# Kernel tuning notes

Measured on AMD Instinct MI355X. Metric: run time of the kernel, lower is better.

## Reference

```python
import jax, jax.numpy as jnp
import numpy as np

H = 1024

def setup_inputs() -> dict:
    key = jax.random.key(0)
    ks = jax.random.split(key, 7)
    s = 1.0 / np.sqrt(H)
    return {
        "hidden_states": jax.random.normal(ks[0], (4, 2048, H), dtype=jnp.float32),
        "Wq": jax.random.uniform(ks[1], (H, H), jnp.float32, -s, s),
        "bq": jax.random.uniform(ks[2], (H,), jnp.float32, -s, s),
        "Wk": jax.random.uniform(ks[3], (H, H), jnp.float32, -s, s),
        "bk": jax.random.uniform(ks[4], (H,), jnp.float32, -s, s),
        "Wv": jax.random.uniform(ks[5], (H, H), jnp.float32, -s, s),
        "bv": jax.random.uniform(ks[6], (H,), jnp.float32, -s, s),
    }

def reference(hidden_states, Wq, bq, Wk, bk, Wv, bv):
    # Linear projections (torch Linear: x @ W.T + b)
    q = hidden_states @ Wq.T + bq  # [B,S,H]
    k = hidden_states @ Wk.T + bk
    v = hidden_states @ Wv.T + bv
    # Unscaled attention
    probs = jax.nn.softmax(jnp.einsum("bqh,bkh->bqk", q, k), axis=-1)  # [B,S,S]
    attention_scores = jnp.sum(probs, axis=-2)  # [B,S] column sums
    context = jnp.einsum("bqk,bkh->bqh", probs, v)  # [B,S,H]
    return (context, attention_scores)
```

## Files before the change

### kernel.cpp

```cpp
#include <hip/hip_runtime.h>
#include <stdint.h>


typedef __attribute__((ext_vector_type(8))) short short8;
typedef __attribute__((ext_vector_type(4))) float floatx4;
typedef __attribute__((ext_vector_type(4))) unsigned short ushort4v;
typedef __attribute__((ext_vector_type(8))) unsigned short ushort8v;
typedef unsigned short u16;

__device__ __forceinline__ u16 f2bf(float f) {
  union { float f; uint32_t u; } v; v.f = f;
  uint32_t u = v.u;
  return (u16)((u + 0x7FFFu + ((u >> 16) & 1u)) >> 16);
}
__device__ __forceinline__ float bf2f(u16 h) {
  union { uint32_t u; float f; } v; v.u = ((uint32_t)h) << 16; return v.f;
}

#define AS3(p) ((__attribute__((address_space(3))) void*)(uint32_t)(uintptr_t)(p))
#define AS1(p) ((__attribute__((address_space(1))) void*)(uintptr_t)(p))

__global__ __launch_bounds__(256) void cvt_all_kernel(
    const float* __restrict__ hs, const float* __restrict__ Wq,
    const float* __restrict__ Wk, const float* __restrict__ Wv,
    u16* __restrict__ hsb, u16* __restrict__ Wb, float* __restrict__ lsum) {
  const int bx = blockIdx.x;
  const float* src;
  u16* dst;
  int i;
  if (bx < 4096) {
    i = bx * 2048 + threadIdx.x * 8;
    src = hs; dst = hsb;
  } else {
    const int idx = bx - 4096;
    const int p = idx >> 9, blk = idx & 511;
    src = (p == 0) ? Wq : (p == 1) ? Wk : Wv;
    dst = Wb + p * 1048576;
    i = blk * 2048 + threadIdx.x * 8;
  }
  const float4 v0 = *(const float4*)(src + i);
  const float4 v1 = *(const float4*)(src + i + 4);
  ushort8v o;
  o[0] = f2bf(v0.x); o[1] = f2bf(v0.y); o[2] = f2bf(v0.z); o[3] = f2bf(v0.w);
  o[4] = f2bf(v1.x); o[5] = f2bf(v1.y); o[6] = f2bf(v1.z); o[7] = f2bf(v1.w);
  *(ushort8v*)(dst + i) = o;
  if (bx == 0) {
    float4 z = {0.f, 0.f, 0.f, 0.f};
#pragma unroll
    for (int k = 0; k < 8; ++k)
      *(float4*)(lsum + threadIdx.x * 32 + k * 4) = z;
  }
}

#define DC_SLOTU 24576

template <int NT>
__device__ __forceinline__ void deep_core(const u16* __restrict__ A,
                                          const u16* __restrict__ B,
                                          int lda, int ldb,
                                          u16* smem, floatx4 acc[4][4]) {
  const int tid  = threadIdx.x;
  const int lane = tid & 63;
  const int w    = tid >> 6;
  const int wm   = w >> 1;
  const int wn   = w & 1;
  const int fr   = lane & 15;
  const int quad = lane >> 4;
  const int pc0  = (quad ^ (fr & 7)) * 8;
  const int pc1  = ((4 + quad) ^ (fr & 7)) * 8;

  const u16* pA[4]; uint32_t dA[4];
#pragma unroll
  for (int j = 0; j < 4; ++j) {
    const int c = tid + j * 512, row = c >> 3, kc = c & 7;
    pA[j] = A + row * lda + (kc ^ (row & 7)) * 8;
    dA[j] = c * 8;
  }
  const u16* pB[2]; uint32_t dB[2];
#pragma unroll
  for (int j = 0; j < 2; ++j) {
    const int c = tid + j * 512, row = c >> 3, kc = c & 7;
    pB[j] = B + row * ldb + (kc ^ (row & 7)) * 8;
    dB[j] = 16384 + c * 8;
  }

#define DC_STA(u) do { u16* s_ = smem + ((u) % 3) * DC_SLOTU;                                  \
    _Pragma("unroll") for (int j_ = 0; j_ < 4; ++j_)                                           \
      __builtin_amdgcn_global_load_lds(AS1(pA[j_] + (u) * 64), AS3(s_ + dA[j_]), 16, 0, 0);   \
  } while (0)
#define DC_STB(u) do { u16* s_ = smem + ((u) % 3) * DC_SLOTU;                                  \
    _Pragma("unroll") for (int j_ = 0; j_ < 2; ++j_)                                           \
      __builtin_amdgcn_global_load_lds(AS1(pB[j_] + (u) * 64), AS3(s_ + dB[j_]), 16, 0, 0);   \
  } while (0)

  DC_STA(0); DC_STB(0); DC_STA(1); DC_STB(1);
  asm volatile("s_waitcnt vmcnt(6)" ::: "memory");
  __builtin_amdgcn_s_barrier();

  const int arow0 = wm * 64 + fr;
  const int brow0 = wn * 64 + fr;

#pragma unroll
  for (int t = 0; t < NT; ++t) {
    const u16* sA = smem + (t % 3) * DC_SLOTU;
    const u16* sB = sA + 16384;
    short8 af[4], bf[4];

#pragma unroll
    for (int mi = 0; mi < 4; ++mi)
      af[mi] = *(const short8*)(sA + (arow0 + mi * 16) * 64 + pc0);
#pragma unroll
    for (int ni = 0; ni < 4; ++ni)
      bf[ni] = *(const short8*)(sB + (brow0 + ni * 16) * 64 + pc0);
    if (t < NT - 2) DC_STA(t + 2);
    __builtin_amdgcn_s_barrier();
    asm volatile("s_waitcnt lgkmcnt(0)" ::: "memory");
    __builtin_amdgcn_sched_barrier(0);
    __builtin_amdgcn_s_setprio(1);
#pragma unroll
    for (int mi = 0; mi < 4; ++mi)
#pragma unroll
      for (int ni = 0; ni < 4; ++ni)
        acc[mi][ni] = __builtin_amdgcn_mfma_f32_16x16x32_bf16(af[mi], bf[ni],
                                                              acc[mi][ni], 0, 0, 0);
    __builtin_amdgcn_s_setprio(0);
    __builtin_amdgcn_s_barrier();

#pragma unroll
    for (int mi = 0; mi < 4; ++mi)
      af[mi] = *(const short8*)(sA + (arow0 + mi * 16) * 64 + pc1);
#pragma unroll
    for (int ni = 0; ni < 4; ++ni)
      bf[ni] = *(const short8*)(sB + (brow0 + ni * 16) * 64 + pc1);
    if (t < NT - 2) {
      DC_STB(t + 2);
      asm volatile("s_waitcnt vmcnt(6)" ::: "memory");
    } else if (t == NT - 2) {
      asm volatile("s_waitcnt vmcnt(0)" ::: "memory");
    }
    __builtin_amdgcn_s_barrier();
    asm volatile("s_waitcnt lgkmcnt(0)" ::: "memory");
    __builtin_amdgcn_sched_barrier(0);
    __builtin_amdgcn_s_setprio(1);
#pragma unroll
    for (int mi = 0; mi < 4; ++mi)
#pragma unroll
      for (int ni = 0; ni < 4; ++ni)
        acc[mi][ni] = __builtin_amdgcn_mfma_f32_16x16x32_bf16(af[mi], bf[ni],
                                                              acc[mi][ni], 0, 0, 0);
    __builtin_amdgcn_s_setprio(0);
    __builtin_amdgcn_s_barrier();
  }
#undef DC_STA
#undef DC_STB
}

__global__ __launch_bounds__(512, 2) void proj_deep_kernel(
    const u16* __restrict__ hsb, const u16* __restrict__ Wb,
    const float* __restrict__ bq, const float* __restrict__ bk,
    const float* __restrict__ bv,
    u16* __restrict__ qo, u16* __restrict__ ko, u16* __restrict__ vt) {
  extern __shared__ __align__(16) u16 smem[];
  floatx4 acc[4][4];
#pragma unroll
  for (int i = 0; i < 4; ++i)
#pragma unroll
    for (int j = 0; j < 4; ++j) acc[i][j] = {0.f, 0.f, 0.f, 0.f};

  const int p    = blockIdx.z;
  const int flat = blockIdx.x + blockIdx.y * 8;
  const int swz  = (flat & 7) * 32 + (flat >> 3);
  const int m0   = (swz >> 3) * 256;
  const int n0   = (swz & 7) * 128;

  deep_core<16>(hsb + m0 * 1024, Wb + p * 1048576 + n0 * 1024, 1024, 1024, smem, acc);

  const float* bias = (p == 0) ? bq : (p == 1) ? bk : bv;
  const int lane = threadIdx.x & 63, w = threadIdx.x >> 6;
  const int wm = w >> 1, wn = w & 1;
  const int fr = lane & 15, rg4 = (lane >> 4) * 4;

  if (p < 2) {
    u16* out = (p == 0) ? qo : ko;
#pragma unroll
    for (int mi = 0; mi < 4; ++mi)
#pragma unroll
      for (int ni = 0; ni < 4; ++ni) {
        const int n = n0 + wn * 64 + ni * 16 + fr;
        const float bn = bias[n];
#pragma unroll
        for (int r = 0; r < 4; ++r) {
          const int m = m0 + wm * 64 + mi * 16 + rg4 + r;
          out[m * 1024 + n] = f2bf(acc[mi][ni][r] + bn);
        }
      }
  } else {
#pragma unroll
    for (int mi = 0; mi < 4; ++mi) {
      const int mbase = m0 + wm * 64 + mi * 16 + rg4;
      const int b = mbase >> 11, s = mbase & 2047;
#pragma unroll
      for (int ni = 0; ni < 4; ++ni) {
        const int n = n0 + wn * 64 + ni * 16 + fr;
        const float bn = bias[n];
        ushort4v pk;
#pragma unroll
        for (int r = 0; r < 4; ++r) pk[r] = f2bf(acc[mi][ni][r] + bn);
        *(ushort4v*)(vt + b * 2097152 + n * 2048 + s) = pk;
      }
    }
  }
}

__global__ __launch_bounds__(512, 2) void logits_q4_kernel(
    const u16* __restrict__ q, const u16* __restrict__ k,
    u16* __restrict__ E, float* __restrict__ lsum) {
  extern __shared__ __align__(16) u16 smem[];
  const int tid  = threadIdx.x;
  const int lane = tid & 63;
  const int w    = tid >> 6;
  const int wr4  = w >> 2;
  const int wc4  = w & 3;
  const int fr   = lane & 15;
  const int kq   = lane >> 4;
  const int pc0  = (kq ^ (fr & 7)) * 8;
  const int pc1  = ((4 + kq) ^ (fr & 7)) * 8;

  const int flat = blockIdx.x + blockIdx.y * 8 + blockIdx.z * 64;
  const int swz  = (flat & 7) * 32 + (flat >> 3);
  const int b    = swz >> 6;
  const int m0   = ((swz >> 3) & 7) * 256;
  const int n0   = (swz & 7) * 256;

  const u16* Ag = q + (b * 2048 + m0) * 1024;
  const u16* Bg = k + (b * 2048 + n0) * 1024;

  const u16* pAs[2]; const u16* pBs[2]; uint32_t dof[2];
#pragma unroll
  for (int j = 0; j < 2; ++j) {
    const int c = tid + j * 512, rl = c >> 3, kc = c & 7;
    const int gc = (kc ^ (rl & 7)) * 8;
    pAs[j] = Ag + rl * 1024 + gc;
    pBs[j] = Bg + rl * 1024 + gc;
    dof[j] = c * 8;
  }
#define ST_A(h, tt, sbase) do { _Pragma("unroll") for (int j_ = 0; j_ < 2; ++j_)      \
    __builtin_amdgcn_global_load_lds(AS1(pAs[j_] + (h) * 131072 + (tt) * 64),         \
        AS3(smem + (sbase) + (h) * 8192 + dof[j_]), 16, 0, 0); } while (0)
#define ST_B(h, tt, sbase) do { _Pragma("unroll") for (int j_ = 0; j_ < 2; ++j_)      \
    __builtin_amdgcn_global_load_lds(AS1(pBs[j_] + (h) * 131072 + (tt) * 64),         \
        AS3(smem + (sbase) + 16384 + (h) * 8192 + dof[j_]), 16, 0, 0); } while (0)

  floatx4 acc[2][2][4][2];
#pragma unroll
  for (int i = 0; i < 2; ++i)
#pragma unroll
    for (int j = 0; j < 2; ++j)
#pragma unroll
      for (int mi = 0; mi < 4; ++mi)
#pragma unroll
        for (int ni = 0; ni < 2; ++ni) acc[i][j][mi][ni] = {0.f, 0.f, 0.f, 0.f};

  ST_A(0, 0, 0); ST_B(0, 0, 0); ST_B(1, 0, 0); ST_A(1, 0, 0);
  asm volatile("s_waitcnt vmcnt(4)" ::: "memory");
  __builtin_amdgcn_s_barrier();

  const int ar0 = wr4 * 64 + fr;
  const int br0 = wc4 * 32 + fr;
  short8 af[4][2], bf[2][2];

#define Q4_READ_A(ah) do { _Pragma("unroll") for (int mi = 0; mi < 4; ++mi) {          \
    af[mi][0] = *(const short8*)(sA + ((ah) * 128 + ar0 + mi * 16) * 64 + pc0);        \
    af[mi][1] = *(const short8*)(sA + ((ah) * 128 + ar0 + mi * 16) * 64 + pc1); } } while (0)
#define Q4_READ_B(bh) do { _Pragma("unroll") for (int ni = 0; ni < 2; ++ni) {          \
    bf[ni][0] = *(const short8*)(sB + ((bh) * 128 + br0 + ni * 16) * 64 + pc0);        \
    bf[ni][1] = *(const short8*)(sB + ((bh) * 128 + br0 + ni * 16) * 64 + pc1); } } while (0)
#define Q4_MFMA(ah, bh) do {                                                           \
    __builtin_amdgcn_s_barrier();                                                      \
    asm volatile("s_waitcnt lgkmcnt(0)" ::: "memory");                                 \
    __builtin_amdgcn_sched_barrier(0);                                                 \
    __builtin_amdgcn_s_setprio(1);                                                     \
    _Pragma("unroll") for (int mi = 0; mi < 4; ++mi)                                   \
      _Pragma("unroll") for (int ni = 0; ni < 2; ++ni)                                 \
        _Pragma("unroll") for (int ks = 0; ks < 2; ++ks)                               \
          acc[ah][bh][mi][ni] = __builtin_amdgcn_mfma_f32_16x16x32_bf16(               \
              af[mi][ks], bf[ni][ks], acc[ah][bh][mi][ni], 0, 0, 0);                   \
    __builtin_amdgcn_s_setprio(0);                                                     \
    __builtin_amdgcn_s_barrier(); } while (0)

  for (int t = 0; t < 15; ++t) {
    const uint32_t sb = (uint32_t)(t & 1) * 32768u;
    const uint32_t sn = (uint32_t)((t + 1) & 1) * 32768u;
    const u16* sA = smem + sb;
    const u16* sB = sA + 16384;

    Q4_READ_A(0); Q4_READ_B(0);
    ST_A(0, t + 1, sn);
    asm volatile("s_waitcnt vmcnt(4)" ::: "memory");
    Q4_MFMA(0, 0);
    Q4_READ_B(1);
    ST_B(0, t + 1, sn);
    asm volatile("s_waitcnt vmcnt(4)" ::: "memory");
    Q4_MFMA(0, 1);
    Q4_READ_A(1); Q4_READ_B(0);
    ST_B(1, t + 1, sn);
    Q4_MFMA(1, 0);
    Q4_READ_B(1);
    ST_A(1, t + 1, sn);
    asm volatile("s_waitcnt vmcnt(4)" ::: "memory");
    Q4_MFMA(1, 1);
  }

  {
    const u16* sA = smem + 32768;
    const u16* sB = sA + 16384;
    Q4_READ_A(0); Q4_READ_B(0);
    asm volatile("s_waitcnt vmcnt(2)" ::: "memory");
    Q4_MFMA(0, 0);
    Q4_READ_B(1);
    asm volatile("s_waitcnt vmcnt(0)" ::: "memory");
    Q4_MFMA(0, 1);
    Q4_READ_A(1); Q4_READ_B(0);
    Q4_MFMA(1, 0);
    Q4_READ_B(1);
    Q4_MFMA(1, 1);
  }

  u16* Eb = E + b * 4194304;
  float* lb = lsum + b * 2048;
#pragma unroll
  for (int ah = 0; ah < 2; ++ah)
#pragma unroll
    for (int mi = 0; mi < 4; ++mi) {
      floatx4 rs = {0.f, 0.f, 0.f, 0.f};
      const int rbase = m0 + ah * 128 + wr4 * 64 + mi * 16 + kq * 4;
#pragma unroll
      for (int bh = 0; bh < 2; ++bh)
#pragma unroll
        for (int ni = 0; ni < 2; ++ni) {
          const int n = n0 + bh * 128 + wc4 * 32 + ni * 16 + fr;
#pragma unroll
          for (int r = 0; r < 4; ++r) {
            const float e = __expf(acc[ah][bh][mi][ni][r]);
            rs[r] += e;
            Eb[(rbase + r) * 2048 + n] = f2bf(e);
          }
        }
#pragma unroll
      for (int off = 1; off < 16; off <<= 1) {
        rs[0] += __shfl_xor(rs[0], off, 64);
        rs[1] += __shfl_xor(rs[1], off, 64);
        rs[2] += __shfl_xor(rs[2], off, 64);
        rs[3] += __shfl_xor(rs[3], off, 64);
      }
      if (fr == 0) {
#pragma unroll
        for (int r = 0; r < 4; ++r) atomicAdd(&lb[rbase + r], rs[r]);
      }
    }
#undef Q4_READ_A
#undef Q4_READ_B
#undef Q4_MFMA
#undef ST_A
#undef ST_B
}

__global__ __launch_bounds__(512, 2) void context_deep_kernel(
    const u16* __restrict__ E, const u16* __restrict__ vt,
    const float* __restrict__ lsum, float* __restrict__ out) {
  extern __shared__ __align__(16) u16 smem[];
  floatx4 acc[4][4];
#pragma unroll
  for (int i = 0; i < 4; ++i)
#pragma unroll
    for (int j = 0; j < 4; ++j) acc[i][j] = {0.f, 0.f, 0.f, 0.f};

  const int flat = blockIdx.x + blockIdx.y * 8 + blockIdx.z * 64;
  const int swz  = (flat & 7) * 32 + (flat >> 3);
  const int b    = swz >> 6;
  const int m0   = ((swz >> 3) & 7) * 256;
  const int n0   = (swz & 7) * 128;

  deep_core<32>(E + b * 4194304 + m0 * 2048, vt + b * 2097152 + n0 * 2048,
                2048, 2048, smem, acc);

  const int lane = threadIdx.x & 63, w = threadIdx.x >> 6;
  const int wm = w >> 1, wn = w & 1;
  const int fr = lane & 15, rg4 = (lane >> 4) * 4;
  const float* lb = lsum + b * 2048;

#pragma unroll
  for (int mi = 0; mi < 4; ++mi) {
    const int rbase = m0 + wm * 64 + mi * 16 + rg4;
    float rinv[4];
#pragma unroll
    for (int r = 0; r < 4; ++r) rinv[r] = 1.0f / lb[rbase + r];
#pragma unroll
    for (int ni = 0; ni < 4; ++ni) {
      const int n = n0 + wn * 64 + ni * 16 + fr;
#pragma unroll
      for (int r = 0; r < 4; ++r)
        out[(b * 2048 + rbase + r) * 1024 + n] = acc[mi][ni][r] * rinv[r];
    }
  }
}

__global__ __launch_bounds__(256) void colsum_part_kernel(
    const u16* __restrict__ E, const float* __restrict__ lsum,
    float* __restrict__ part) {
  const int b  = blockIdx.x;
  const int g  = blockIdx.y;
  const int q0 = g * 64;
  const int j  = blockIdx.z * 1024 + threadIdx.x * 4;
  const u16* Eb = E + b * 4194304;
  const float* lb = lsum + b * 2048;
  float acc[4];
#pragma unroll
  for (int c = 0; c < 4; ++c) acc[c] = 0.f;
  for (int r = 0; r < 64; ++r) {
    const int qi = q0 + r;
    const float rinv = 1.0f / lb[qi];
    const ushort4v ev = *(const ushort4v*)(Eb + qi * 2048 + j);
#pragma unroll
    for (int c = 0; c < 4; ++c) acc[c] += bf2f((u16)ev[c]) * rinv;
  }
  float4 o = {acc[0], acc[1], acc[2], acc[3]};
  *(float4*)(part + (b * 32 + g) * 2048 + j) = o;
}

__global__ __launch_bounds__(256) void colsum_reduce_kernel(
    const float* __restrict__ part, float* __restrict__ scores) {
  const int b = blockIdx.x;
  const int j = blockIdx.y * 256 + threadIdx.x;
  const float* pb = part + b * 32 * 2048 + j;
  float s = 0.f;
#pragma unroll
  for (int g = 0; g < 32; ++g) s += pb[g * 2048];
  scores[b * 2048 + j] = s;
}

extern "C" void kernel_launch(void* const* d_in, const int* in_sizes, int n_in,
                              void* d_out, int out_size, void* d_ws, size_t ws_size,
                              hipStream_t stream) {
  const float* hs = (const float*)d_in[0];
  const float* Wq = (const float*)d_in[1];
  const float* bq = (const float*)d_in[2];
  const float* Wk = (const float*)d_in[3];
  const float* bk = (const float*)d_in[4];
  const float* Wv = (const float*)d_in[5];
  const float* bv = (const float*)d_in[6];

  char* ws = (char*)d_ws;
  u16*   qw  = (u16*)(ws);
  u16*   kw  = (u16*)(ws + (16u << 20));
  u16*   vtw = (u16*)(ws + (32u << 20));
  float* lw  = (float*)(ws + (48u << 20));
  float* pw  = (float*)(ws + (48u << 20) + (128u << 10));
  u16*   hsb = (u16*)(ws + (49u << 20));
  u16*   Wb  = (u16*)(ws + (65u << 20));
  u16*   Ew  = (u16*)(ws + (49u << 20));

  float* outc = (float*)d_out;
  float* outs = outc + 8388608;

  static int s_attr_done = 0;
  if (!s_attr_done) {
    (void)hipFuncSetAttribute((const void*)proj_deep_kernel,
                              hipFuncAttributeMaxDynamicSharedMemorySize, 147456);
    (void)hipFuncSetAttribute((const void*)logits_q4_kernel,
                              hipFuncAttributeMaxDynamicSharedMemorySize, 131072);
    (void)hipFuncSetAttribute((const void*)context_deep_kernel,
                              hipFuncAttributeMaxDynamicSharedMemorySize, 147456);
    s_attr_done = 1;
  }

  cvt_all_kernel<<<5632, 256, 0, stream>>>(hs, Wq, Wk, Wv, hsb, Wb, lw);
  proj_deep_kernel<<<dim3(8, 32, 3), 512, 147456, stream>>>(hsb, Wb, bq, bk, bv, qw, kw, vtw);
  logits_q4_kernel<<<dim3(8, 8, 4), 512, 131072, stream>>>(qw, kw, Ew, lw);
  context_deep_kernel<<<dim3(8, 8, 4), 512, 147456, stream>>>(Ew, vtw, lw, outc);
  colsum_part_kernel<<<dim3(4, 32, 2), 256, 0, stream>>>(Ew, lw, pw);
  colsum_reduce_kernel<<<dim3(4, 8), 256, 0, stream>>>(pw, outs);
}
```

Measured before the change: 235.8 us.

## Switch QKV projection to 256x256 q4 GEMM core shared with logits kernel

Factors the logits kernel's 256x256-tile GEMM core into a reusable templated q4_core and uses it for the QKV projection, replacing the 256x128 deep_core tile. Larger output tiles halve the number of blocks and raise arithmetic intensity per block (more reuse of loaded A/B tiles). It also changes launch bounds to one block per CU, which may lower occupancy and latency hiding, and the projection grid shrinks to 384 blocks, which may hurt wave-quantization balance.

```diff
diff --git a/kernel.cpp b/kernel.cpp
--- a/kernel.cpp
+++ b/kernel.cpp
@@ -52,170 +52,11 @@
   }
 }
 
-#define DC_SLOTU 24576
-
 template <int NT>
-__device__ __forceinline__ void deep_core(const u16* __restrict__ A,
-                                          const u16* __restrict__ B,
-                                          int lda, int ldb,
-                                          u16* smem, floatx4 acc[4][4]) {
-  const int tid  = threadIdx.x;
-  const int lane = tid & 63;
-  const int w    = tid >> 6;
-  const int wm   = w >> 1;
-  const int wn   = w & 1;
-  const int fr   = lane & 15;
-  const int quad = lane >> 4;
-  const int pc0  = (quad ^ (fr & 7)) * 8;
-  const int pc1  = ((4 + quad) ^ (fr & 7)) * 8;
-
-  const u16* pA[4]; uint32_t dA[4];
-#pragma unroll
-  for (int j = 0; j < 4; ++j) {
-    const int c = tid + j * 512, row = c >> 3, kc = c & 7;
-    pA[j] = A + row * lda + (kc ^ (row & 7)) * 8;
-    dA[j] = c * 8;
-  }
-  const u16* pB[2]; uint32_t dB[2];
-#pragma unroll
-  for (int j = 0; j < 2; ++j) {
-    const int c = tid + j * 512, row = c >> 3, kc = c & 7;
-    pB[j] = B + row * ldb + (kc ^ (row & 7)) * 8;
-    dB[j] = 16384 + c * 8;
-  }
-
-#define DC_STA(u) do { u16* s_ = smem + ((u) % 3) * DC_SLOTU;                                  \
-    _Pragma("unroll") for (int j_ = 0; j_ < 4; ++j_)                                           \
-      __builtin_amdgcn_global_load_lds(AS1(pA[j_] + (u) * 64), AS3(s_ + dA[j_]), 16, 0, 0);   \
-  } while (0)
-#define DC_STB(u) do { u16* s_ = smem + ((u) % 3) * DC_SLOTU;                                  \
-    _Pragma("unroll") for (int j_ = 0; j_ < 2; ++j_)                                           \
-      __builtin_amdgcn_global_load_lds(AS1(pB[j_] + (u) * 64), AS3(s_ + dB[j_]), 16, 0, 0);   \
-  } while (0)
-
-  DC_STA(0); DC_STB(0); DC_STA(1); DC_STB(1);
-  asm volatile("s_waitcnt vmcnt(6)" ::: "memory");
-  __builtin_amdgcn_s_barrier();
-
-  const int arow0 = wm * 64 + fr;
-  const int brow0 = wn * 64 + fr;
-
-#pragma unroll
-  for (int t = 0; t < NT; ++t) {
-    const u16* sA = smem + (t % 3) * DC_SLOTU;
-    const u16* sB = sA + 16384;
-    short8 af[4], bf[4];
-
-#pragma unroll
-    for (int mi = 0; mi < 4; ++mi)
-      af[mi] = *(const short8*)(sA + (arow0 + mi * 16) * 64 + pc0);
-#pragma unroll
-    for (int ni = 0; ni < 4; ++ni)
-      bf[ni] = *(const short8*)(sB + (brow0 + ni * 16) * 64 + pc0);
-    if (t < NT - 2) DC_STA(t + 2);
-    __builtin_amdgcn_s_barrier();
-    asm volatile("s_waitcnt lgkmcnt(0)" ::: "memory");
-    __builtin_amdgcn_sched_barrier(0);
-    __builtin_amdgcn_s_setprio(1);
-#pragma unroll
-    for (int mi = 0; mi < 4; ++mi)
-#pragma unroll
-      for (int ni = 0; ni < 4; ++ni)
-        acc[mi][ni] = __builtin_amdgcn_mfma_f32_16x16x32_bf16(af[mi], bf[ni],
-                                                              acc[mi][ni], 0, 0, 0);
-    __builtin_amdgcn_s_setprio(0);
-    __builtin_amdgcn_s_barrier();
-
-#pragma unroll
-    for (int mi = 0; mi < 4; ++mi)
-      af[mi] = *(const short8*)(sA + (arow0 + mi * 16) * 64 + pc1);
-#pragma unroll
-    for (int ni = 0; ni < 4; ++ni)
-      bf[ni] = *(const short8*)(sB + (brow0 + ni * 16) * 64 + pc1);
-    if (t < NT - 2) {
-      DC_STB(t + 2);
-      asm volatile("s_waitcnt vmcnt(6)" ::: "memory");
-    } else if (t == NT - 2) {
-      asm volatile("s_waitcnt vmcnt(0)" ::: "memory");
-    }
-    __builtin_amdgcn_s_barrier();
-    asm volatile("s_waitcnt lgkmcnt(0)" ::: "memory");
-    __builtin_amdgcn_sched_barrier(0);
-    __builtin_amdgcn_s_setprio(1);
-#pragma unroll
-    for (int mi = 0; mi < 4; ++mi)
-#pragma unroll
-      for (int ni = 0; ni < 4; ++ni)
-        acc[mi][ni] = __builtin_amdgcn_mfma_f32_16x16x32_bf16(af[mi], bf[ni],
-                                                              acc[mi][ni], 0, 0, 0);
-    __builtin_amdgcn_s_setprio(0);
-    __builtin_amdgcn_s_barrier();
-  }
-#undef DC_STA
-#undef DC_STB
-}
-
-__global__ __launch_bounds__(512, 2) void proj_deep_kernel(
-    const u16* __restrict__ hsb, const u16* __restrict__ Wb,
-    const float* __restrict__ bq, const float* __restrict__ bk,
-    const float* __restrict__ bv,
-    u16* __restrict__ qo, u16* __restrict__ ko, u16* __restrict__ vt) {
-  extern __shared__ __align__(16) u16 smem[];
-  floatx4 acc[4][4];
-#pragma unroll
-  for (int i = 0; i < 4; ++i)
-#pragma unroll
-    for (int j = 0; j < 4; ++j) acc[i][j] = {0.f, 0.f, 0.f, 0.f};
-
-  const int p    = blockIdx.z;
-  const int flat = blockIdx.x + blockIdx.y * 8;
-  const int swz  = (flat & 7) * 32 + (flat >> 3);
-  const int m0   = (swz >> 3) * 256;
-  const int n0   = (swz & 7) * 128;
-
-  deep_core<16>(hsb + m0 * 1024, Wb + p * 1048576 + n0 * 1024, 1024, 1024, smem, acc);
-
-  const float* bias = (p == 0) ? bq : (p == 1) ? bk : bv;
-  const int lane = threadIdx.x & 63, w = threadIdx.x >> 6;
-  const int wm = w >> 1, wn = w & 1;
-  const int fr = lane & 15, rg4 = (lane >> 4) * 4;
-
-  if (p < 2) {
-    u16* out = (p == 0) ? qo : ko;
-#pragma unroll
-    for (int mi = 0; mi < 4; ++mi)
-#pragma unroll
-      for (int ni = 0; ni < 4; ++ni) {
-        const int n = n0 + wn * 64 + ni * 16 + fr;
-        const float bn = bias[n];
-#pragma unroll
-        for (int r = 0; r < 4; ++r) {
-          const int m = m0 + wm * 64 + mi * 16 + rg4 + r;
-          out[m * 1024 + n] = f2bf(acc[mi][ni][r] + bn);
-        }
-      }
-  } else {
-#pragma unroll
-    for (int mi = 0; mi < 4; ++mi) {
-      const int mbase = m0 + wm * 64 + mi * 16 + rg4;
-      const int b = mbase >> 11, s = mbase & 2047;
-#pragma unroll
-      for (int ni = 0; ni < 4; ++ni) {
-        const int n = n0 + wn * 64 + ni * 16 + fr;
-        const float bn = bias[n];
-        ushort4v pk;
-#pragma unroll
-        for (int r = 0; r < 4; ++r) pk[r] = f2bf(acc[mi][ni][r] + bn);
-        *(ushort4v*)(vt + b * 2097152 + n * 2048 + s) = pk;
-      }
-    }
-  }
-}
-
-__global__ __launch_bounds__(512, 2) void logits_q4_kernel(
-    const u16* __restrict__ q, const u16* __restrict__ k,
-    u16* __restrict__ E, float* __restrict__ lsum) {
-  extern __shared__ __align__(16) u16 smem[];
+__device__ __forceinline__ void q4_core(const u16* __restrict__ A,
+                                        const u16* __restrict__ B,
+                                        int lda, int ldb,
+                                        u16* smem, floatx4 acc[2][2][4][2]) {
   const int tid  = threadIdx.x;
   const int lane = tid & 63;
   const int w    = tid >> 6;
@@ -226,40 +67,21 @@
   const int pc0  = (kq ^ (fr & 7)) * 8;
   const int pc1  = ((4 + kq) ^ (fr & 7)) * 8;
 
-  const int flat = blockIdx.x + blockIdx.y * 8 + blockIdx.z * 64;
-  const int swz  = (flat & 7) * 32 + (flat >> 3);
-  const int b    = swz >> 6;
-  const int m0   = ((swz >> 3) & 7) * 256;
-  const int n0   = (swz & 7) * 256;
-
-  const u16* Ag = q + (b * 2048 + m0) * 1024;
-  const u16* Bg = k + (b * 2048 + n0) * 1024;
-
   const u16* pAs[2]; const u16* pBs[2]; uint32_t dof[2];
 #pragma unroll
   for (int j = 0; j < 2; ++j) {
     const int c = tid + j * 512, rl = c >> 3, kc = c & 7;
     const int gc = (kc ^ (rl & 7)) * 8;
-    pAs[j] = Ag + rl * 1024 + gc;
-    pBs[j] = Bg + rl * 1024 + gc;
+    pAs[j] = A + rl * lda + gc;
+    pBs[j] = B + rl * ldb + gc;
     dof[j] = c * 8;
   }
 #define ST_A(h, tt, sbase) do { _Pragma("unroll") for (int j_ = 0; j_ < 2; ++j_)      \
-    __builtin_amdgcn_global_load_lds(AS1(pAs[j_] + (h) * 131072 + (tt) * 64),         \
+    __builtin_amdgcn_global_load_lds(AS1(pAs[j_] + (h) * 128 * lda + (tt) * 64),      \
         AS3(smem + (sbase) + (h) * 8192 + dof[j_]), 16, 0, 0); } while (0)
 #define ST_B(h, tt, sbase) do { _Pragma("unroll") for (int j_ = 0; j_ < 2; ++j_)      \
-    __builtin_amdgcn_global_load_lds(AS1(pBs[j_] + (h) * 131072 + (tt) * 64),         \
+    __builtin_amdgcn_global_load_lds(AS1(pBs[j_] + (h) * 128 * ldb + (tt) * 64),      \
         AS3(smem + (sbase) + 16384 + (h) * 8192 + dof[j_]), 16, 0, 0); } while (0)
-
-  floatx4 acc[2][2][4][2];
-#pragma unroll
-  for (int i = 0; i < 2; ++i)
-#pragma unroll
-    for (int j = 0; j < 2; ++j)
-#pragma unroll
-      for (int mi = 0; mi < 4; ++mi)
-#pragma unroll
-        for (int ni = 0; ni < 2; ++ni) acc[i][j][mi][ni] = {0.f, 0.f, 0.f, 0.f};
 
   ST_A(0, 0, 0); ST_B(0, 0, 0); ST_B(1, 0, 0); ST_A(1, 0, 0);
   asm volatile("s_waitcnt vmcnt(4)" ::: "memory");
@@ -288,7 +110,7 @@
     __builtin_amdgcn_s_setprio(0);                                                     \
     __builtin_amdgcn_s_barrier(); } while (0)
 
-  for (int t = 0; t < 15; ++t) {
+  for (int t = 0; t < NT - 1; ++t) {
     const uint32_t sb = (uint32_t)(t & 1) * 32768u;
     const uint32_t sn = (uint32_t)((t + 1) & 1) * 32768u;
     const u16* sA = smem + sb;
@@ -312,7 +134,7 @@
   }
 
   {
-    const u16* sA = smem + 32768;
+    const u16* sA = smem + (uint32_t)((NT - 1) & 1) * 32768u;
     const u16* sB = sA + 16384;
     Q4_READ_A(0); Q4_READ_B(0);
     asm volatile("s_waitcnt vmcnt(2)" ::: "memory");
@@ -325,9 +147,111 @@
     Q4_READ_B(1);
     Q4_MFMA(1, 1);
   }
-
+#undef Q4_READ_A
+#undef Q4_READ_B
+#undef Q4_MFMA
+#undef ST_A
+#undef ST_B
+}
+
+__global__ __launch_bounds__(512, 1) void proj_q4_kernel(
+    const u16* __restrict__ hsb, const u16* __restrict__ Wb,
+    const float* __restrict__ bq, const float* __restrict__ bk,
+    const float* __restrict__ bv,
+    u16* __restrict__ qo, u16* __restrict__ ko, u16* __restrict__ vt) {
+  extern __shared__ __align__(16) u16 smem[];
+  floatx4 acc[2][2][4][2];
+#pragma unroll
+  for (int i = 0; i < 2; ++i)
+#pragma unroll
+    for (int j = 0; j < 2; ++j)
+#pragma unroll
+      for (int mi = 0; mi < 4; ++mi)
+#pragma unroll
+        for (int ni = 0; ni < 2; ++ni) acc[i][j][mi][ni] = {0.f, 0.f, 0.f, 0.f};
+
+  const int p    = blockIdx.z;
+  const int flat = blockIdx.x + blockIdx.y * 4;
+  const int swz  = (flat & 7) * 16 + (flat >> 3);
+  const int m0   = (swz >> 2) * 256;
+  const int n0   = (swz & 3) * 256;
+
+  q4_core<16>(hsb + m0 * 1024, Wb + p * 1048576 + n0 * 1024, 1024, 1024, smem, acc);
+
+  const float* bias = (p == 0) ? bq : (p == 1) ? bk : bv;
+  const int lane = threadIdx.x & 63, w = threadIdx.x >> 6;
+  const int wr4 = w >> 2, wc4 = w & 3;
+  const int fr = lane & 15, kq = lane >> 4;
+
+  if (p < 2) {
+    u16* out = (p == 0) ? qo : ko;
+#pragma unroll
+    for (int ah = 0; ah < 2; ++ah)
+#pragma unroll
+      for (int mi = 0; mi < 4; ++mi) {
+        const int mb = m0 + ah * 128 + wr4 * 64 + mi * 16 + kq * 4;
+#pragma unroll
+        for (int bh = 0; bh < 2; ++bh)
+#pragma unroll
+          for (int ni = 0; ni < 2; ++ni) {
+            const int n = n0 + bh * 128 + wc4 * 32 + ni * 16 + fr;
+            const float bn = bias[n];
+#pragma unroll
+            for (int r = 0; r < 4; ++r)
+              out[(mb + r) * 1024 + n] = f2bf(acc[ah][bh][mi][ni][r] + bn);
+          }
+      }
+  } else {
+#pragma unroll
+    for (int ah = 0; ah < 2; ++ah)
+#pragma unroll
+      for (int mi = 0; mi < 4; ++mi) {
+        const int mbase = m0 + ah * 128 + wr4 * 64 + mi * 16 + kq * 4;
+        const int b = mbase >> 11, s = mbase & 2047;
+#pragma unroll
+        for (int bh = 0; bh < 2; ++bh)
+#pragma unroll
+          for (int ni = 0; ni < 2; ++ni) {
+            const int n = n0 + bh * 128 + wc4 * 32 + ni * 16 + fr;
+            const float bn = bias[n];
+            ushort4v pk;
+#pragma unroll
+            for (int r = 0; r < 4; ++r) pk[r] = f2bf(acc[ah][bh][mi][ni][r] + bn);
+            *(ushort4v*)(vt + b * 2097152 + n * 2048 + s) = pk;
+          }
+      }
+  }
+}
+
+__global__ __launch_bounds__(512, 1) void logits_q4_kernel(
+    const u16* __restrict__ q, const u16* __restrict__ k,
+    u16* __restrict__ E, float* __restrict__ lsum) {
+  extern __shared__ __align__(16) u16 smem[];
+  floatx4 acc[2][2][4][2];
+#pragma unroll
+  for (int i = 0; i < 2; ++i)
+#pragma unroll
+    for (int j = 0; j < 2; ++j)
+#pragma unroll
+      for (int mi = 0; mi < 4; ++mi)
+#pragma unroll
+        for (int ni = 0; ni < 2; ++ni) acc[i][j][mi][ni] = {0.f, 0.f, 0.f, 0.f};
+
+  const int flat = blockIdx.x + blockIdx.y * 8 + blockIdx.z * 64;
+  const int swz  = (flat & 7) * 32 + (flat >> 3);
+  const int b    = swz >> 6;
+  const int m0   = ((swz >> 3) & 7) * 256;
+  const int n0   = (swz & 7) * 256;
+
+  q4_core<16>(q + (b * 2048 + m0) * 1024, k + (b * 2048 + n0) * 1024,
+              1024, 1024, smem, acc);
+
+  const int lane = threadIdx.x & 63, w = threadIdx.x >> 6;
+  const int wr4 = w >> 2, wc4 = w & 3;
+  const int fr = lane & 15, kq = lane >> 4;
   u16* Eb = E + b * 4194304;
   float* lb = lsum + b * 2048;
+
 #pragma unroll
   for (int ah = 0; ah < 2; ++ah)
 #pragma unroll
@@ -358,11 +282,109 @@
         for (int r = 0; r < 4; ++r) atomicAdd(&lb[rbase + r], rs[r]);
       }
     }
-#undef Q4_READ_A
-#undef Q4_READ_B
-#undef Q4_MFMA
-#undef ST_A
-#undef ST_B
+}
+
+#define DC_SLOTU 24576
+
+template <int NT>
+__device__ __forceinline__ void deep_core(const u16* __restrict__ A,
+                                          const u16* __restrict__ B,
+                                          int lda, int ldb,
+                                          u16* smem, floatx4 acc[4][4]) {
+  const int tid  = threadIdx.x;
+  const int lane = tid & 63;
+  const int w    = tid >> 6;
+  const int wm   = w >> 1;
+  const int wn   = w & 1;
+  const int fr   = lane & 15;
+  const int quad = lane >> 4;
+  const int pc0  = (quad ^ (fr & 7)) * 8;
+  const int pc1  = ((4 + quad) ^ (fr & 7)) * 8;
+
+  const u16* pA[4]; uint32_t dA[4];
+#pragma unroll
+  for (int j = 0; j < 4; ++j) {
+    const int c = tid + j * 512, row = c >> 3, kc = c & 7;
+    pA[j] = A + row * lda + (kc ^ (row & 7)) * 8;
+    dA[j] = c * 8;
+  }
+  const u16* pB[2]; uint32_t dB[2];
+#pragma unroll
+  for (int j = 0; j < 2; ++j) {
+    const int c = tid + j * 512, row = c >> 3, kc = c & 7;
+    pB[j] = B + row * ldb + (kc ^ (row & 7)) * 8;
+    dB[j] = 16384 + c * 8;
+  }
+
+#define DC_STA(u) do { u16* s_ = smem + ((u) % 3) * DC_SLOTU;                                  \
+    _Pragma("unroll") for (int j_ = 0; j_ < 4; ++j_)                                           \
+      __builtin_amdgcn_global_load_lds(AS1(pA[j_] + (u) * 64), AS3(s_ + dA[j_]), 16, 0, 0);   \
+  } while (0)
+#define DC_STB(u) do { u16* s_ = smem + ((u) % 3) * DC_SLOTU;                                  \
+    _Pragma("unroll") for (int j_ = 0; j_ < 2; ++j_)                                           \
+      __builtin_amdgcn_global_load_lds(AS1(pB[j_] + (u) * 64), AS3(s_ + dB[j_]), 16, 0, 0);   \
+  } while (0)
+
+  DC_STA(0); DC_STB(0); DC_STA(1); DC_STB(1);
+  asm volatile("s_waitcnt vmcnt(6)" ::: "memory");
+  __builtin_amdgcn_s_barrier();
+
+  const int arow0 = wm * 64 + fr;
+  const int brow0 = wn * 64 + fr;
+
+#pragma unroll
+  for (int t = 0; t < NT; ++t) {
+    const u16* sA = smem + (t % 3) * DC_SLOTU;
+    const u16* sB = sA + 16384;
+    short8 af[4], bf[4];
+
+#pragma unroll
+    for (int mi = 0; mi < 4; ++mi)
+      af[mi] = *(const short8*)(sA + (arow0 + mi * 16) * 64 + pc0);
+#pragma unroll
+    for (int ni = 0; ni < 4; ++ni)
+      bf[ni] = *(const short8*)(sB + (brow0 + ni * 16) * 64 + pc0);
+    if (t < NT - 2) DC_STA(t + 2);
+    __builtin_amdgcn_s_barrier();
+    asm volatile("s_waitcnt lgkmcnt(0)" ::: "memory");
+    __builtin_amdgcn_sched_barrier(0);
+    __builtin_amdgcn_s_setprio(1);
+#pragma unroll
+    for (int mi = 0; mi < 4; ++mi)
+#pragma unroll
+      for (int ni = 0; ni < 4; ++ni)
+        acc[mi][ni] = __builtin_amdgcn_mfma_f32_16x16x32_bf16(af[mi], bf[ni],
+                                                              acc[mi][ni], 0, 0, 0);
+    __builtin_amdgcn_s_setprio(0);
+    __builtin_amdgcn_s_barrier();
+
+#pragma unroll
+    for (int mi = 0; mi < 4; ++mi)
+      af[mi] = *(const short8*)(sA + (arow0 + mi * 16) * 64 + pc1);
+#pragma unroll
+    for (int ni = 0; ni < 4; ++ni)
+      bf[ni] = *(const short8*)(sB + (brow0 + ni * 16) * 64 + pc1);
+    if (t < NT - 2) {
+      DC_STB(t + 2);
+      asm volatile("s_waitcnt vmcnt(6)" ::: "memory");
+    } else if (t == NT - 2) {
+      asm volatile("s_waitcnt vmcnt(0)" ::: "memory");
+    }
+    __builtin_amdgcn_s_barrier();
+    asm volatile("s_waitcnt lgkmcnt(0)" ::: "memory");
+    __builtin_amdgcn_sched_barrier(0);
+    __builtin_amdgcn_s_setprio(1);
+#pragma unroll
+    for (int mi = 0; mi < 4; ++mi)
+#pragma unroll
+      for (int ni = 0; ni < 4; ++ni)
+        acc[mi][ni] = __builtin_amdgcn_mfma_f32_16x16x32_bf16(af[mi], bf[ni],
+                                                              acc[mi][ni], 0, 0, 0);
+    __builtin_amdgcn_s_setprio(0);
+    __builtin_amdgcn_s_barrier();
+  }
+#undef DC_STA
+#undef DC_STB
 }
 
 __global__ __launch_bounds__(512, 2) void context_deep_kernel(
@@ -465,8 +487,8 @@
 
   static int s_attr_done = 0;
   if (!s_attr_done) {
-    (void)hipFuncSetAttribute((const void*)proj_deep_kernel,
-                              hipFuncAttributeMaxDynamicSharedMemorySize, 147456);
+    (void)hipFuncSetAttribute((const void*)proj_q4_kernel,
+                              hipFuncAttributeMaxDynamicSharedMemorySize, 131072);
     (void)hipFuncSetAttribute((const void*)logits_q4_kernel,
                               hipFuncAttributeMaxDynamicSharedMemorySize, 131072);
     (void)hipFuncSetAttribute((const void*)context_deep_kernel,
@@ -475,7 +497,7 @@
   }
 
   cvt_all_kernel<<<5632, 256, 0, stream>>>(hs, Wq, Wk, Wv, hsb, Wb, lw);
-  proj_deep_kernel<<<dim3(8, 32, 3), 512, 147456, stream>>>(hsb, Wb, bq, bk, bv, qw, kw, vtw);
+  proj_q4_kernel<<<dim3(4, 32, 3), 512, 131072, stream>>>(hsb, Wb, bq, bk, bv, qw, kw, vtw);
   logits_q4_kernel<<<dim3(8, 8, 4), 512, 131072, stream>>>(qw, kw, Ew, lw);
   context_deep_kernel<<<dim3(8, 8, 4), 512, 147456, stream>>>(Ew, vtw, lw, outc);
   colsum_part_kernel<<<dim3(4, 32, 2), 256, 0, stream>>>(Ew, lw, pw);
```

Result: slower. 252.7 us (+7.1%).
